# Kernel optimization log

Hardware: AMD Instinct MI355X
Metric: run time of the kernel (lower is better)

## Reference

```python
import jax, jax.numpy as jnp
import numpy as np

HEADS = 8
N_NODES = 16384
DIM = 256
NUM_GLOBAL = 4
E_LOCAL = 131072
E_EXP = 65536


def setup_inputs() -> dict:
    key = jax.random.key(0)
    ks = jax.random.split(key, 8)
    x = jax.random.normal(ks[0], (N_NODES, DIM), dtype=jnp.float32)
    edge_index = jax.random.randint(ks[1], (2, E_LOCAL), 0, N_NODES)
    expander_edge_index = jax.random.randint(ks[2], (2, E_EXP), 0, N_NODES)
    W_qkv = jax.random.normal(ks[3], (DIM, 3 * DIM), dtype=jnp.float32) * (DIM ** -0.5)
    b_qkv = jax.random.normal(ks[4], (3 * DIM,), dtype=jnp.float32) * 0.01
    W_out = jax.random.normal(ks[5], (DIM, DIM), dtype=jnp.float32) * (DIM ** -0.5)
    b_out = jax.random.normal(ks[6], (DIM,), dtype=jnp.float32) * 0.01
    global_tokens = jax.random.normal(ks[7], (NUM_GLOBAL, DIM), dtype=jnp.float32)
    return {"x": x, "edge_index": edge_index,
            "expander_edge_index": expander_edge_index,
            "W_qkv": W_qkv, "b_qkv": b_qkv,
            "W_out": W_out, "b_out": b_out,
            "global_tokens": global_tokens}


def _build_edges(edge_index, expander_edge_index, N, G):
    # local edges + self loops (PyG add_self_loops appends [i,i] edges)
    self_loops = jnp.arange(N)
    nodes = jnp.arange(N)
    gids = jnp.arange(N, N + G)
    # node -> global: meshgrid(arange(N), global_nodes, 'ij') -> src node repeated, dst global tiled
    n2g_src = jnp.repeat(nodes, G)
    n2g_dst = jnp.tile(gids, N)
    src = jnp.concatenate([edge_index[0], self_loops, expander_edge_index[0], n2g_src, n2g_dst])
    dst = jnp.concatenate([edge_index[1], self_loops, expander_edge_index[1], n2g_dst, n2g_src])
    return src, dst


def reference(x, edge_index, expander_edge_index, W_qkv, b_qkv, W_out, b_out, global_tokens):
    N, dim = x.shape
    G = global_tokens.shape[0]
    H = HEADS
    D = dim // H
    total = N + G

    x_full = jnp.concatenate([x, global_tokens], axis=0)          # [N+G, dim]
    qkv = (x_full @ W_qkv + b_qkv).reshape(total, 3, H, D)
    Q, K, V = qkv[:, 0], qkv[:, 1], qkv[:, 2]                     # [N+G, H, D]

    src, dst = _build_edges(edge_index, expander_edge_index, N, G)  # [E]

    scale = D ** -0.5
    scores = (Q[dst] * K[src]).sum(axis=-1) * scale               # [E, H]

    # segment softmax over destination nodes
    m = jax.ops.segment_max(scores, dst, num_segments=total)      # [N+G, H]
    e = jnp.exp(scores - m[dst])                                  # [E, H]
    denom = jax.ops.segment_sum(e, dst, num_segments=total)       # [N+G, H]
    attn = e / denom[dst]                                         # [E, H]

    # scatter-weighted V sum (index_add over dst)
    out = jax.ops.segment_sum(attn[:, :, None] * V[src], dst, num_segments=total)  # [N+G, H, D]
    out = out[:N].reshape(N, H * D)
    return out @ W_out + b_out
```

## Files before the change

### kernel.cpp

```cpp
#include <hip/hip_runtime.h>
#include <hip/hip_bf16.h>
#include <stdint.h>

#define N_NODES   16384
#define DIMM      256
#define HEADS     8
#define HDIM      32
#define NUM_GLOBAL 4
#define N_TOT     (N_NODES + NUM_GLOBAL)
#define E_LOCAL   131072
#define E_EXP     65536
#define E_CSR     (E_LOCAL + E_EXP)
#define ADJ_CAP   64

typedef __hip_bfloat16 bf16;
typedef __attribute__((ext_vector_type(8))) short short8;
typedef __attribute__((ext_vector_type(8))) unsigned short ush8;
typedef __attribute__((ext_vector_type(4))) short sh4;
typedef __attribute__((ext_vector_type(4))) float f32x4;

__device__ __forceinline__ short f2s(float f) {
    bf16 h = __float2bfloat16(f);
    return __builtin_bit_cast(short, h);
}
__device__ __forceinline__ float bu2f(unsigned short u) {
    return __bfloat162float(__builtin_bit_cast(bf16, u));
}

__device__ __forceinline__ int swz(int c, int r) {
    return c ^ (r & 7) ^ ((r >> 3) & 7);
}

__global__ __launch_bounds__(256) void prep_kernel(
    const float* __restrict__ Wqkv, const float* __restrict__ Wout,
    const float* __restrict__ x, const float* __restrict__ gtok,
    bf16* __restrict__ Wt1, bf16* __restrict__ Wt2,
    int* __restrict__ cnt, bf16* __restrict__ Xb)
{
    const int b = blockIdx.x;
    const int t = threadIdx.x;
    if (b < 64) {
        __shared__ float T[64][65];
        const float* src; bf16* dst; int n0, k0, ldn;
        if (b < 48) { src = Wqkv; dst = Wt1; n0 = (b % 12) * 64; k0 = (b / 12) * 64; ldn = 768; }
        else        { int bb = b - 48; src = Wout; dst = Wt2; n0 = (bb & 3) * 64; k0 = (bb >> 2) * 64; ldn = 256; }
        #pragma unroll
        for (int i = 0; i < 4; ++i) {
            int idx = t + 256 * i;
            int r = idx >> 4, c4 = (idx & 15) * 4;
            float4 v = *(const float4*)(src + (size_t)(k0 + r) * ldn + n0 + c4);
            T[r][c4] = v.x; T[r][c4 + 1] = v.y; T[r][c4 + 2] = v.z; T[r][c4 + 3] = v.w;
        }
        __syncthreads();
        #pragma unroll
        for (int i = 0; i < 4; ++i) {
            int idx = t + 256 * i;
            int nr = idx >> 4, kk = (idx & 15) * 4;
            sh4 o;
            o[0] = f2s(T[kk][nr]);     o[1] = f2s(T[kk + 1][nr]);
            o[2] = f2s(T[kk + 2][nr]); o[3] = f2s(T[kk + 3][nr]);
            *(sh4*)(dst + (size_t)(n0 + nr) * 256 + k0 + kk) = o;
        }
    } else {
        if (b < 80) {
            ((int4*)cnt)[(b - 64) * 256 + t] = make_int4(0, 0, 0, 0);
        }
        int e0 = ((b - 64) * 256 + t) * 8;
        if (e0 < N_TOT * DIMM) {
            int row = e0 >> 8, col = e0 & 255;
            const float* p = (row < N_NODES)
                ? x + (size_t)row * DIMM + col
                : gtok + (size_t)(row - N_NODES) * DIMM + col;
            float4 v0 = *(const float4*)p, v1 = *(const float4*)(p + 4);
            short8 o;
            o[0] = f2s(v0.x); o[1] = f2s(v0.y); o[2] = f2s(v0.z); o[3] = f2s(v0.w);
            o[4] = f2s(v1.x); o[5] = f2s(v1.y); o[6] = f2s(v1.z); o[7] = f2s(v1.w);
            *(short8*)((short*)Xb + (size_t)row * DIMM + col) = o;
        }
    }
}

__global__ __launch_bounds__(256) void qkv_mfma(
    const bf16* __restrict__ Xb, const bf16* __restrict__ Wt,
    const float* __restrict__ bias,
    const int* __restrict__ ei, const int* __restrict__ xei,
    int* __restrict__ cnt, unsigned short* __restrict__ adjP,
    bf16* __restrict__ Qb, bf16* __restrict__ KVp)
{
    const int braw = blockIdx.x;
    const int t  = threadIdx.x;
    if (braw < 768) {
        int e = braw * 256 + t;
        int s, d;
        if (e < E_LOCAL) { s = ei[e];            d = ei[E_LOCAL + e]; }
        else             { int ee = e - E_LOCAL; s = xei[ee]; d = xei[E_EXP + ee]; }
        int pos = atomicAdd(&cnt[d], 1);
        if (pos < ADJ_CAP) adjP[(d << 6) + pos] = (unsigned short)s;
        return;
    }
    const int b = braw - 768;
    const int xcd = b & 7;
    const int i = b >> 3;
    const int mt = xcd + 8 * (i / 6);
    if (mt >= 129) return;
    const int m0 = mt * 128;
    const int n0 = (i % 6) * 128;

    __shared__ __align__(16) short SM[128 * 136];
    short* As = SM;
    short* Bs = SM + 8192;
    const int wid = t >> 6, lane = t & 63;
    const int wr = wid >> 1, wc = wid & 1;
    const int lm = lane & 15, lq = lane >> 4;

    f32x4 acc[4][4] = {};
    short8 aregs[4], bregs[4];

    int sr[4], skc[4];
    #pragma unroll
    for (int ii = 0; ii < 4; ++ii) {
        int c8 = t + 256 * ii;
        sr[ii] = c8 >> 3; skc[ii] = c8 & 7;
    }

    #pragma unroll
    for (int ii = 0; ii < 4; ++ii) {
        aregs[ii] = *(const short8*)((const short*)Xb + (size_t)(m0 + sr[ii]) * DIMM + skc[ii] * 8);
        bregs[ii] = *(const short8*)((const short*)Wt + (size_t)(n0 + sr[ii]) * 256 + skc[ii] * 8);
    }
    #pragma unroll
    for (int ii = 0; ii < 4; ++ii) {
        *(short8*)(As + sr[ii] * 64 + swz(skc[ii], sr[ii]) * 8) = aregs[ii];
        *(short8*)(Bs + sr[ii] * 64 + swz(skc[ii], sr[ii]) * 8) = bregs[ii];
    }
    __syncthreads();

    #pragma unroll
    for (int tstep = 0; tstep < 4; ++tstep) {
        if (tstep < 3) {
            const int kn = (tstep + 1) * 64;
            #pragma unroll
            for (int ii = 0; ii < 4; ++ii) {
                aregs[ii] = *(const short8*)((const short*)Xb + (size_t)(m0 + sr[ii]) * DIMM + kn + skc[ii] * 8);
                bregs[ii] = *(const short8*)((const short*)Wt + (size_t)(n0 + sr[ii]) * 256 + kn + skc[ii] * 8);
            }
        }
        #pragma unroll
        for (int kk = 0; kk < 2; ++kk) {
            const int c = kk * 4 + lq;
            short8 af[4], bfq[4];
            #pragma unroll
            for (int mi = 0; mi < 4; ++mi) {
                int r = wr * 64 + mi * 16 + lm;
                af[mi] = *(const short8*)(As + r * 64 + swz(c, r) * 8);
            }
            #pragma unroll
            for (int ni = 0; ni < 4; ++ni) {
                int n = wc * 64 + ni * 16 + lm;
                bfq[ni] = *(const short8*)(Bs + n * 64 + swz(c, n) * 8);
            }
            #pragma unroll
            for (int mi = 0; mi < 4; ++mi)
                #pragma unroll
                for (int ni = 0; ni < 4; ++ni)
                    acc[mi][ni] = __builtin_amdgcn_mfma_f32_16x16x32_bf16(
                        af[mi], bfq[ni], acc[mi][ni], 0, 0, 0);
        }
        if (tstep < 3) {
            __syncthreads();
            #pragma unroll
            for (int ii = 0; ii < 4; ++ii) {
                *(short8*)(As + sr[ii] * 64 + swz(skc[ii], sr[ii]) * 8) = aregs[ii];
                *(short8*)(Bs + sr[ii] * 64 + swz(skc[ii], sr[ii]) * 8) = bregs[ii];
            }
            __syncthreads();
        }
    }

    __syncthreads();
    #pragma unroll
    for (int ni = 0; ni < 4; ++ni) {
        int col = wc * 64 + ni * 16 + lm;
        float bv = bias[n0 + col];
        #pragma unroll
        for (int mi = 0; mi < 4; ++mi) {
            int rowb = wr * 64 + mi * 16 + lq * 4;
            #pragma unroll
            for (int rr = 0; rr < 4; ++rr)
                SM[(rowb + rr) * 136 + col] = f2s(acc[mi][ni][rr] + bv);
        }
    }
    __syncthreads();
    #pragma unroll
    for (int it = 0; it < 8; ++it) {
        int idx = it * 256 + t;
        int r = idx >> 4, c8 = idx & 15;
        int row = m0 + r;
        if (row < N_TOT) {
            int colbase = n0 + (c8 >> 3) * 64;
            int sel = colbase >> 8;
            int cc = (colbase & 255) + (c8 & 7) * 8;
            short8 v = *(const short8*)(SM + r * 136 + c8 * 8);
            short* dp;
            if (sel == 0) {
                dp = (short*)Qb + (size_t)row * DIMM + cc;
            } else {
                int head = cc >> 5, dim = cc & 31;
                int pr = head >> 1, sub = head & 1;
                dp = (short*)KVp + ((size_t)pr * N_TOT + row) * 128
                   + (sel - 1) * 64 + sub * 32 + dim;
            }
            *(short8*)dp = v;
        }
    }
}

__global__ __launch_bounds__(256) void out_mfma(
    const bf16* __restrict__ O, const bf16* __restrict__ Wt,
    const float* __restrict__ bias, float* __restrict__ out)
{
    const int b = blockIdx.x;
    const int xcd = b & 7;
    const int i = b >> 3;
    const int m0 = (xcd + 8 * (i >> 1)) * 128;
    const int n0 = (i & 1) * 128;

    __shared__ __align__(16) short SM[128 * 136];
    short* As = SM;
    short* Bs = SM + 8192;
    float* CF = (float*)SM;
    const int t  = threadIdx.x;
    const int wid = t >> 6, lane = t & 63;
    const int wr = wid >> 1, wc = wid & 1;
    const int lm = lane & 15, lq = lane >> 4;

    f32x4 acc[4][4] = {};
    short8 aregs[4], bregs[4];

    int sr[4], skc[4];
    #pragma unroll
    for (int ii = 0; ii < 4; ++ii) {
        int c8 = t + 256 * ii;
        sr[ii] = c8 >> 3; skc[ii] = c8 & 7;
    }

    #pragma unroll
    for (int ii = 0; ii < 4; ++ii) {
        aregs[ii] = *(const short8*)((const short*)O + (size_t)(m0 + sr[ii]) * DIMM + skc[ii] * 8);
        bregs[ii] = *(const short8*)((const short*)Wt + (size_t)(n0 + sr[ii]) * 256 + skc[ii] * 8);
    }
    #pragma unroll
    for (int ii = 0; ii < 4; ++ii) {
        *(short8*)(As + sr[ii] * 64 + swz(skc[ii], sr[ii]) * 8) = aregs[ii];
        *(short8*)(Bs + sr[ii] * 64 + swz(skc[ii], sr[ii]) * 8) = bregs[ii];
    }
    __syncthreads();

    #pragma unroll
    for (int tstep = 0; tstep < 4; ++tstep) {
        if (tstep < 3) {
            const int kn = (tstep + 1) * 64;
            #pragma unroll
            for (int ii = 0; ii < 4; ++ii) {
                aregs[ii] = *(const short8*)((const short*)O + (size_t)(m0 + sr[ii]) * DIMM + kn + skc[ii] * 8);
                bregs[ii] = *(const short8*)((const short*)Wt + (size_t)(n0 + sr[ii]) * 256 + kn + skc[ii] * 8);
            }
        }
        #pragma unroll
        for (int kk = 0; kk < 2; ++kk) {
            const int c = kk * 4 + lq;
            short8 af[4], bfq[4];
            #pragma unroll
            for (int mi = 0; mi < 4; ++mi) {
                int r = wr * 64 + mi * 16 + lm;
                af[mi] = *(const short8*)(As + r * 64 + swz(c, r) * 8);
            }
            #pragma unroll
            for (int ni = 0; ni < 4; ++ni) {
                int n = wc * 64 + ni * 16 + lm;
                bfq[ni] = *(const short8*)(Bs + n * 64 + swz(c, n) * 8);
            }
            #pragma unroll
            for (int mi = 0; mi < 4; ++mi)
                #pragma unroll
                for (int ni = 0; ni < 4; ++ni)
                    acc[mi][ni] = __builtin_amdgcn_mfma_f32_16x16x32_bf16(
                        af[mi], bfq[ni], acc[mi][ni], 0, 0, 0);
        }
        if (tstep < 3) {
            __syncthreads();
            #pragma unroll
            for (int ii = 0; ii < 4; ++ii) {
                *(short8*)(As + sr[ii] * 64 + swz(skc[ii], sr[ii]) * 8) = aregs[ii];
                *(short8*)(Bs + sr[ii] * 64 + swz(skc[ii], sr[ii]) * 8) = bregs[ii];
            }
            __syncthreads();
        }
    }

    #pragma unroll
    for (int p = 0; p < 2; ++p) {
        __syncthreads();
        if (wr == p) {
            #pragma unroll
            for (int ni = 0; ni < 4; ++ni) {
                int col = wc * 64 + ni * 16 + lm;
                float bv = bias[n0 + col];
                #pragma unroll
                for (int mi = 0; mi < 4; ++mi) {
                    int lr = mi * 16 + lq * 4;
                    #pragma unroll
                    for (int rr = 0; rr < 4; ++rr) {
                        float val = acc[mi][ni][rr] + bv;
                        val = fminf(fmaxf(val, -1e4f), 1e4f);
                        CF[(lr + rr) * 132 + col] = val;
                    }
                }
            }
        }
        __syncthreads();
        #pragma unroll
        for (int it = 0; it < 8; ++it) {
            int idx = it * 256 + t;
            int r = idx >> 5, c4 = idx & 31;
            float4 v = *(const float4*)(CF + r * 132 + c4 * 4);
            *(float4*)(out + (size_t)(m0 + p * 64 + r) * DIMM + n0 + c4 * 4) = v;
        }
    }
}

__global__ __launch_bounds__(256) void attn_kernel(
    const bf16* __restrict__ Qb, const bf16* __restrict__ KVp,
    const int* __restrict__ cnt, const unsigned short* __restrict__ adjP,
    bf16* __restrict__ Ob)
{
    const int b = blockIdx.x;
    const int pair = b & 3;
    const int wid = threadIdx.x >> 6;
    const int lane = threadIdx.x & 63;
    const int n = (b >> 2) * 4 + wid;
    const int g = lane >> 3, j = lane & 7;
    const float scale = 0.1767766952966369f;

    const unsigned short* KV = (const unsigned short*)KVp + (size_t)pair * N_TOT * 128;

    const int hoff = (pair * 2 + (j >> 2)) * 32 + (j & 3) * 8;
    ush8 qu = *(const ush8*)((const unsigned short*)Qb + (size_t)n * DIMM + hoff);
    float qf[8];
    #pragma unroll
    for (int e = 0; e < 8; ++e) qf[e] = bu2f(qu[e]) * scale;

    const int areg = adjP[(n << 6) + lane];
    const int deg = min(cnt[n], ADJ_CAP);
    const int tot = deg + 5;

    float acc[8] = {0.f, 0.f, 0.f, 0.f, 0.f, 0.f, 0.f, 0.f};
    float dsum = 0.f;

    auto IDX = [&](int base, int& sv, float& ok) {
        int ii = base + g - 5;
        bool val = (ii < deg);
        int sg = __shfl(areg, ii & 63);
        int s  = (ii < 0) ? ((ii == -5) ? n : (N_NODES + ii + 4)) : sg;
        sv = val ? s : n;
        ok = val ? 1.f : 0.f;
    };

    int svA; float okA;
    IDX(0, svA, okA);
    ush8 kA = *(const ush8*)(KV + (size_t)svA * 128 + j * 8);
    ush8 vA = *(const ush8*)(KV + (size_t)svA * 128 + 64 + j * 8);

    int base = 0;
    while (true) {
        int svB; float okB; ush8 kB, vB;
        const bool more = (base + 8 < tot);
        if (more) {
            IDX(base + 8, svB, okB);
            kB = *(const ush8*)(KV + (size_t)svB * 128 + j * 8);
            vB = *(const ush8*)(KV + (size_t)svB * 128 + 64 + j * 8);
        }
        {
            float p = qf[0] * bu2f(kA[0]) + qf[1] * bu2f(kA[1])
                    + qf[2] * bu2f(kA[2]) + qf[3] * bu2f(kA[3])
                    + qf[4] * bu2f(kA[4]) + qf[5] * bu2f(kA[5])
                    + qf[6] * bu2f(kA[6]) + qf[7] * bu2f(kA[7]);
            p += __shfl_xor(p, 1);
            p += __shfl_xor(p, 2);
            float wgt = okA * __expf(fminf(p, 80.f));
            dsum += wgt;
            #pragma unroll
            for (int e = 0; e < 8; ++e) acc[e] += wgt * bu2f(vA[e]);
        }
        if (!more) break;
        base += 8;
        svA = svB; okA = okB; kA = kB; vA = vB;
    }

    #pragma unroll
    for (int m = 8; m <= 32; m <<= 1) {
        #pragma unroll
        for (int e = 0; e < 8; ++e) acc[e] += __shfl_xor(acc[e], m);
        dsum += __shfl_xor(dsum, m);
    }

    if (g == 0) {
        float r = 1.0f / fmaxf(dsum, 1e-30f);
        ush8 o;
        #pragma unroll
        for (int e = 0; e < 8; ++e) {
            float v = fminf(fmaxf(acc[e] * r, -500.f), 500.f);
            o[e] = (unsigned short)__builtin_bit_cast(short, __float2bfloat16(v));
        }
        *(ush8*)((unsigned short*)Ob + (size_t)n * DIMM + hoff) = o;
    }
}

extern "C" void kernel_launch(void* const* d_in, const int* in_sizes, int n_in,
                              void* d_out, int out_size, void* d_ws, size_t ws_size,
                              hipStream_t stream)
{
    const float* x    = (const float*)d_in[0];
    const int*   ei   = (const int*)d_in[1];
    const int*   xei  = (const int*)d_in[2];
    const float* Wqkv = (const float*)d_in[3];
    const float* bqkv = (const float*)d_in[4];
    const float* Wout = (const float*)d_in[5];
    const float* bout = (const float*)d_in[6];
    const float* gtok = (const float*)d_in[7];

    int* cnt  = (int*)d_ws;
    unsigned short* adjP = (unsigned short*)(cnt + N_NODES);
    uintptr_t fb = ((uintptr_t)(adjP + (size_t)N_NODES * ADJ_CAP) + 15) & ~(uintptr_t)15;
    bf16*  Qb  = (bf16*)fb;
    bf16*  KVp = Qb + (size_t)N_TOT * DIMM;
    bf16*  Ob  = KVp + (size_t)N_TOT * 512;
    bf16*  Wt1 = Ob + (size_t)N_NODES * DIMM;
    bf16*  Wt2 = Wt1 + 768 * 256;
    bf16*  Xb  = Wt2 + 256 * 256;

    prep_kernel<<<2113, 256, 0, stream>>>(Wqkv, Wout, x, gtok, Wt1, Wt2, cnt, Xb);
    qkv_mfma<<<768 + 816, 256, 0, stream>>>(Xb, Wt1, bqkv, ei, xei, cnt, adjP, Qb, KVp);
    attn_kernel<<<(N_NODES / 4) * 4, 256, 0, stream>>>(Qb, KVp, cnt, adjP, Ob);
    out_mfma<<<256, 256, 0, stream>>>(Ob, Wt2, bout, (float*)d_out);
}
```

Before: 144.1 us.

## Fuse fp32-to-bf16 input conversion into QKV GEMM loads and use bf16 dot2 for scores

Drops the separate pass that converted x and the global tokens to a bf16 buffer in the prep kernel. The QKV GEMM now reads fp32 rows directly and converts them in registers while staging tiles, which removes one full write and re-read of the activations. The attention kernel computes q·k with the fdot2 bf16 intrinsic when the compiler provides it and applies the scale after the reduction. In exchange the GEMM loads twice as many bytes for the A operand and does the conversion inside its load loop.

Result: slower. 148.1 us (+2.7%).

```diff
diff --git a/kernel.cpp b/kernel.cpp
--- a/kernel.cpp
+++ b/kernel.cpp
@@ -19,6 +19,18 @@
 typedef __attribute__((ext_vector_type(4))) short sh4;
 typedef __attribute__((ext_vector_type(4))) float f32x4;
 
+#if defined(__has_builtin)
+#  if __has_builtin(__builtin_amdgcn_fdot2_f32_bf16)
+#    define HAVE_FDOT2 1
+#  endif
+#endif
+#ifndef HAVE_FDOT2
+#  define HAVE_FDOT2 0
+#endif
+#if HAVE_FDOT2
+typedef __attribute__((ext_vector_type(2))) __bf16 bf16x2;
+#endif
+
 __device__ __forceinline__ short f2s(float f) {
     bf16 h = __float2bfloat16(f);
     return __builtin_bit_cast(short, h);
@@ -33,9 +45,7 @@
 
 __global__ __launch_bounds__(256) void prep_kernel(
     const float* __restrict__ Wqkv, const float* __restrict__ Wout,
-    const float* __restrict__ x, const float* __restrict__ gtok,
-    bf16* __restrict__ Wt1, bf16* __restrict__ Wt2,
-    int* __restrict__ cnt, bf16* __restrict__ Xb)
+    bf16* __restrict__ Wt1, bf16* __restrict__ Wt2, int* __restrict__ cnt)
 {
     const int b = blockIdx.x;
     const int t = threadIdx.x;
@@ -62,27 +72,13 @@
             *(sh4*)(dst + (size_t)(n0 + nr) * 256 + k0 + kk) = o;
         }
     } else {
-        if (b < 80) {
-            ((int4*)cnt)[(b - 64) * 256 + t] = make_int4(0, 0, 0, 0);
-        }
-        int e0 = ((b - 64) * 256 + t) * 8;
-        if (e0 < N_TOT * DIMM) {
-            int row = e0 >> 8, col = e0 & 255;
-            const float* p = (row < N_NODES)
-                ? x + (size_t)row * DIMM + col
-                : gtok + (size_t)(row - N_NODES) * DIMM + col;
-            float4 v0 = *(const float4*)p, v1 = *(const float4*)(p + 4);
-            short8 o;
-            o[0] = f2s(v0.x); o[1] = f2s(v0.y); o[2] = f2s(v0.z); o[3] = f2s(v0.w);
-            o[4] = f2s(v1.x); o[5] = f2s(v1.y); o[6] = f2s(v1.z); o[7] = f2s(v1.w);
-            *(short8*)((short*)Xb + (size_t)row * DIMM + col) = o;
-        }
+        ((int4*)cnt)[(b - 64) * 256 + t] = make_int4(0, 0, 0, 0);
     }
 }
 
 __global__ __launch_bounds__(256) void qkv_mfma(
-    const bf16* __restrict__ Xb, const bf16* __restrict__ Wt,
-    const float* __restrict__ bias,
+    const float* __restrict__ x, const float* __restrict__ gtok,
+    const bf16* __restrict__ Wt, const float* __restrict__ bias,
     const int* __restrict__ ei, const int* __restrict__ xei,
     int* __restrict__ cnt, unsigned short* __restrict__ adjP,
     bf16* __restrict__ Qb, bf16* __restrict__ KVp)
@@ -123,9 +119,25 @@
         sr[ii] = c8 >> 3; skc[ii] = c8 & 7;
     }
 
-    #pragma unroll
-    for (int ii = 0; ii < 4; ++ii) {
-        aregs[ii] = *(const short8*)((const short*)Xb + (size_t)(m0 + sr[ii]) * DIMM + skc[ii] * 8);
+    auto loadA = [&](int ii, int kn) -> short8 {
+        int row = m0 + sr[ii];
+        float4 v0 = make_float4(0.f, 0.f, 0.f, 0.f), v1 = v0;
+        if (row < N_NODES) {
+            const float* p = x + (size_t)row * DIMM + kn + skc[ii] * 8;
+            v0 = *(const float4*)p; v1 = *(const float4*)(p + 4);
+        } else if (row < N_TOT) {
+            const float* p = gtok + (size_t)(row - N_NODES) * DIMM + kn + skc[ii] * 8;
+            v0 = *(const float4*)p; v1 = *(const float4*)(p + 4);
+        }
+        short8 o;
+        o[0] = f2s(v0.x); o[1] = f2s(v0.y); o[2] = f2s(v0.z); o[3] = f2s(v0.w);
+        o[4] = f2s(v1.x); o[5] = f2s(v1.y); o[6] = f2s(v1.z); o[7] = f2s(v1.w);
+        return o;
+    };
+
+    #pragma unroll
+    for (int ii = 0; ii < 4; ++ii) {
+        aregs[ii] = loadA(ii, 0);
         bregs[ii] = *(const short8*)((const short*)Wt + (size_t)(n0 + sr[ii]) * 256 + skc[ii] * 8);
     }
     #pragma unroll
@@ -141,7 +153,7 @@
             const int kn = (tstep + 1) * 64;
             #pragma unroll
             for (int ii = 0; ii < 4; ++ii) {
-                aregs[ii] = *(const short8*)((const short*)Xb + (size_t)(m0 + sr[ii]) * DIMM + kn + skc[ii] * 8);
+                aregs[ii] = loadA(ii, kn);
                 bregs[ii] = *(const short8*)((const short*)Wt + (size_t)(n0 + sr[ii]) * 256 + kn + skc[ii] * 8);
             }
         }
@@ -346,9 +358,13 @@
 
     const int hoff = (pair * 2 + (j >> 2)) * 32 + (j & 3) * 8;
     ush8 qu = *(const ush8*)((const unsigned short*)Qb + (size_t)n * DIMM + hoff);
+#if HAVE_FDOT2
+    const uint4 qw = __builtin_bit_cast(uint4, qu);
+#else
     float qf[8];
     #pragma unroll
-    for (int e = 0; e < 8; ++e) qf[e] = bu2f(qu[e]) * scale;
+    for (int e = 0; e < 8; ++e) qf[e] = bu2f(qu[e]);
+#endif
 
     const int areg = adjP[(n << 6) + lane];
     const int deg = min(cnt[n], ADJ_CAP);
@@ -366,6 +382,26 @@
         ok = val ? 1.f : 0.f;
     };
 
+    auto SCORE = [&](const ush8& kk) -> float {
+#if HAVE_FDOT2
+        uint4 kw = __builtin_bit_cast(uint4, kk);
+        float p = __builtin_amdgcn_fdot2_f32_bf16(
+            __builtin_bit_cast(bf16x2, qw.x), __builtin_bit_cast(bf16x2, kw.x), 0.f, false);
+        p = __builtin_amdgcn_fdot2_f32_bf16(
+            __builtin_bit_cast(bf16x2, qw.y), __builtin_bit_cast(bf16x2, kw.y), p, false);
+        p = __builtin_amdgcn_fdot2_f32_bf16(
+            __builtin_bit_cast(bf16x2, qw.z), __builtin_bit_cast(bf16x2, kw.z), p, false);
+        p = __builtin_amdgcn_fdot2_f32_bf16(
+            __builtin_bit_cast(bf16x2, qw.w), __builtin_bit_cast(bf16x2, kw.w), p, false);
+        return p;
+#else
+        return qf[0] * bu2f(kk[0]) + qf[1] * bu2f(kk[1])
+             + qf[2] * bu2f(kk[2]) + qf[3] * bu2f(kk[3])
+             + qf[4] * bu2f(kk[4]) + qf[5] * bu2f(kk[5])
+             + qf[6] * bu2f(kk[6]) + qf[7] * bu2f(kk[7]);
+#endif
+    };
+
     int svA; float okA;
     IDX(0, svA, okA);
     ush8 kA = *(const ush8*)(KV + (size_t)svA * 128 + j * 8);
@@ -381,13 +417,10 @@
             vB = *(const ush8*)(KV + (size_t)svB * 128 + 64 + j * 8);
         }
         {
-            float p = qf[0] * bu2f(kA[0]) + qf[1] * bu2f(kA[1])
-                    + qf[2] * bu2f(kA[2]) + qf[3] * bu2f(kA[3])
-                    + qf[4] * bu2f(kA[4]) + qf[5] * bu2f(kA[5])
-                    + qf[6] * bu2f(kA[6]) + qf[7] * bu2f(kA[7]);
+            float p = SCORE(kA);
             p += __shfl_xor(p, 1);
             p += __shfl_xor(p, 2);
-            float wgt = okA * __expf(fminf(p, 80.f));
+            float wgt = okA * __expf(fminf(p * scale, 80.f));
             dsum += wgt;
             #pragma unroll
             for (int e = 0; e < 8; ++e) acc[e] += wgt * bu2f(vA[e]);
@@ -437,10 +470,9 @@
     bf16*  Ob  = KVp + (size_t)N_TOT * 512;
     bf16*  Wt1 = Ob + (size_t)N_NODES * DIMM;
     bf16*  Wt2 = Wt1 + 768 * 256;
-    bf16*  Xb  = Wt2 + 256 * 256;
-
-    prep_kernel<<<2113, 256, 0, stream>>>(Wqkv, Wout, x, gtok, Wt1, Wt2, cnt, Xb);
-    qkv_mfma<<<768 + 816, 256, 0, stream>>>(Xb, Wt1, bqkv, ei, xei, cnt, adjP, Qb, KVp);
+
+    prep_kernel<<<80, 256, 0, stream>>>(Wqkv, Wout, Wt1, Wt2, cnt);
+    qkv_mfma<<<768 + 816, 256, 0, stream>>>(x, gtok, Wt1, bqkv, ei, xei, cnt, adjP, Qb, KVp);
     attn_kernel<<<(N_NODES / 4) * 4, 256, 0, stream>>>(Qb, KVp, cnt, adjP, Ob);
     out_mfma<<<256, 256, 0, stream>>>(Ob, Wt2, bout, (float*)d_out);
 }
```
